# Optimization experiments

Measured on AMD Instinct MI355X. Metric: run time of the kernel, lower is better.

## Reference

```python
import jax, jax.numpy as jnp
import numpy as np

# hypers
R_CUT = 5.0      # 'cutoff radius'
N_MAX = 8        # radial channels
L_MAX = 3        # max spherical-harmonic degree
N_ATOMS = 20000
N_PAIRS = 500000
N_SPECIES = 4    # len(all_species)
N_PSEUDO = 2     # 'alchemical'


def setup_inputs() -> dict:
    key = jax.random.key(0)
    k1, k2, k3, k4, k5 = jax.random.split(key, 5)
    positions = jax.random.normal(k1, (N_ATOMS, 3), dtype=jnp.float32) * 2.0
    centers = jax.random.randint(k2, (N_PAIRS,), 0, N_ATOMS)
    neighbors = jax.random.randint(k3, (N_PAIRS,), 0, N_ATOMS)
    species_idx = jax.random.randint(k4, (N_ATOMS,), 0, N_SPECIES).astype(jnp.int32)
    W_comb = jax.random.normal(k5, (N_PSEUDO, N_SPECIES), dtype=jnp.float32)
    return {"positions": positions, "W_comb": W_comb, "centers": centers,
            "neighbors": neighbors, "species_idx": species_idx}


def _real_spherical_harmonics(x, y, z):
    """Real spherical harmonics Y_lm on unit vectors, l = 0..3.
    Returns list of arrays, each [P, 2l+1] ordered m = -l..l."""
    x2, y2, z2 = x * x, y * y, z * z
    Y0 = jnp.full_like(x, 0.28209479177387814)[:, None]
    c1 = 0.4886025119029199
    Y1 = jnp.stack([c1 * y, c1 * z, c1 * x], axis=-1)
    Y2 = jnp.stack([
        1.0925484305920792 * x * y,
        1.0925484305920792 * y * z,
        0.31539156525252005 * (3.0 * z2 - 1.0),
        1.0925484305920792 * x * z,
        0.5462742152960396 * (x2 - y2),
    ], axis=-1)
    Y3 = jnp.stack([
        0.5900435899266435 * y * (3.0 * x2 - y2),
        2.890611442640554 * x * y * z,
        0.4570457994644658 * y * (5.0 * z2 - 1.0),
        0.3731763325901154 * z * (5.0 * z2 - 3.0),
        0.4570457994644658 * x * (5.0 * z2 - 1.0),
        1.445305721320277 * z * (x2 - y2),
        0.5900435899266435 * x * (x2 - 3.0 * y2),
    ], axis=-1)
    return [Y0, Y1, Y2, Y3]


def reference(positions, W_comb, centers, neighbors, species_idx):
    # pairwise displacement vectors (gather over neighbor list)
    vec = positions[neighbors] - positions[centers]            # [P, 3]
    r = jnp.sqrt((vec * vec).sum(-1) + 1e-12)                  # [P]
    u = vec / r[:, None]                                       # unit vectors

    # smooth radial basis with cosine cutoff (Gaussians on a grid)
    fc = jnp.where(r < R_CUT, 0.5 * (jnp.cos(jnp.pi * r / R_CUT) + 1.0), 0.0)
    cn = jnp.linspace(0.0, R_CUT, N_MAX, dtype=positions.dtype)
    sigma = R_CUT / N_MAX
    radial = jnp.exp(-0.5 * ((r[:, None] - cn) / sigma) ** 2) * fc[:, None]  # [P, n]

    # alchemical combination: one_hot(species_neighbor) @ W_comb.T -> [P, q]
    w = W_comb.T[species_idx[neighbors]]                       # [P, q]
    feat = w[:, :, None] * radial[:, None, :]                  # [P, q, n]

    sph = _real_spherical_harmonics(u[:, 0], u[:, 1], u[:, 2])

    blocks = []
    for Yl in sph:
        # per-pair outer product: [P, 2l+1, q, n]
        exp_l = Yl[:, :, None, None] * feat[:, None, :, :]
        # sum over neighbors j for each center i (scatter-add)
        summed = jax.ops.segment_sum(exp_l, centers, num_segments=N_ATOMS)
        blocks.append(summed.reshape(N_ATOMS, Yl.shape[1], N_PSEUDO * N_MAX))
    # concatenate all l blocks along the component (m) axis: [N_atoms, 16, q*n]
    return jnp.concatenate(blocks, axis=1)
```

## Files before the change

### kernel.cpp

```cpp
#include <hip/hip_runtime.h>
#include <math.h>

#define N_SPECIES 4
#define NMAX      8
#define RCUT      5.0f
#define CAP        64
#define CNT_STRIDE 16


__global__ void prep_kernel(const float* __restrict__ pos,
                            const int*  __restrict__ species,
                            float4* __restrict__ posw, int N) {
    int i = blockIdx.x * blockDim.x + threadIdx.x;
    if (i < N) {
        posw[i] = make_float4(pos[3 * i], pos[3 * i + 1], pos[3 * i + 2],
                              __int_as_float(species[i]));
    }
}


__global__ void build_kernel(const int* __restrict__ centers,
                             const int* __restrict__ neighbors,
                             int* __restrict__ cnt,
                             int* __restrict__ bin, int P) {
    int p = blockIdx.x * blockDim.x + threadIdx.x;
    if (p < P) {
        int c = centers[p];
        int j = neighbors[p];
        int idx = atomicAdd(&cnt[c * CNT_STRIDE], 1);
        if (idx < CAP) bin[c * CAP + idx] = j;
    }
}


__global__ __launch_bounds__(64) void accum_kernel(
        const float4* __restrict__ posw,
        const float*  __restrict__ W,
        const int*    __restrict__ cnt,
        const int*    __restrict__ bin,
        float* __restrict__ out, int N) {
    const int i    = blockIdx.x;
    const int lane = threadIdx.x;

    __shared__ __align__(16) float sY[64][20];
    __shared__ __align__(16) float sF[64][20];

    int payload = bin[i * CAP + lane];
    int ci = cnt[i * CNT_STRIDE];
    if (ci > CAP) ci = CAP;
    int j = payload;
    if ((unsigned)j >= (unsigned)N) j = 0;
    float4 pj = posw[j];
    float4 pi = posw[i];

    float dx = pj.x - pi.x, dy = pj.y - pi.y, dz = pj.z - pi.z;
    float r  = sqrtf(dx * dx + dy * dy + dz * dz + 1e-12f);
    float inv = 1.0f / r;
    float x = dx * inv, y = dy * inv, z = dz * inv;

    float fc = (r < RCUT) ? 0.5f * (cosf(3.14159265358979323846f * (r / RCUT)) + 1.0f)
                          : 0.0f;

    const float Ck[NMAX] = {
        1.0f,          5.2045002e-1f, 7.3369700e-2f, 2.8016300e-3f,
        2.8977800e-5f, 8.1185700e-8f, 6.1609600e-11f, 1.2664166e-14f };
    float rc = (r < RCUT) ? r : RCUT;
    float A  = expf(-1.28f * r * r) * fc;
    float B  = expf(1.82857143f * rc);

    int s = __float_as_int(pj.w);
    float w0 = W[s];
    float w1 = W[N_SPECIES + s];

    float f0[NMAX];
    float pw = A;
    #pragma unroll
    for (int k = 0; k < NMAX; ++k) { f0[k] = pw * Ck[k]; pw *= B; }

    if (lane < ci) {
        float* Fr = sF[lane];
        ((float4*)Fr)[0] = make_float4(w0 * f0[0], w0 * f0[1], w0 * f0[2], w0 * f0[3]);
        ((float4*)Fr)[1] = make_float4(w0 * f0[4], w0 * f0[5], w0 * f0[6], w0 * f0[7]);
        ((float4*)Fr)[2] = make_float4(w1 * f0[0], w1 * f0[1], w1 * f0[2], w1 * f0[3]);
        ((float4*)Fr)[3] = make_float4(w1 * f0[4], w1 * f0[5], w1 * f0[6], w1 * f0[7]);

        float x2 = x * x, y2 = y * y, z2 = z * z;
        float* Yr = sY[lane];
        ((float4*)Yr)[0] = make_float4(
            0.28209479177387814f,
            0.4886025119029199f * y,
            0.4886025119029199f * z,
            0.4886025119029199f * x);
        ((float4*)Yr)[1] = make_float4(
            1.0925484305920792f * x * y,
            1.0925484305920792f * y * z,
            0.31539156525252005f * (3.0f * z2 - 1.0f),
            1.0925484305920792f * x * z);
        ((float4*)Yr)[2] = make_float4(
            0.5462742152960396f * (x2 - y2),
            0.5900435899266435f * y * (3.0f * x2 - y2),
            2.890611442640554f  * x * y * z,
            0.4570457994644658f * y * (5.0f * z2 - 1.0f));
        ((float4*)Yr)[3] = make_float4(
            0.3731763325901154f * z * (5.0f * z2 - 3.0f),
            0.4570457994644658f * x * (5.0f * z2 - 1.0f),
            1.445305721320277f  * z * (x2 - y2),
            0.5900435899266435f * x * (x2 - 3.0f * y2));
    }
    __syncthreads();

    const int m  = lane >> 2;
    const int cg = lane & 3;
    float ax = 0.f, ay = 0.f, az = 0.f, aw = 0.f;
    #pragma unroll 4
    for (int l = 0; l < ci; ++l) {
        float yv = sY[l][m];
        float4 f = *(const float4*)&sF[l][cg * 4];
        ax = fmaf(yv, f.x, ax);
        ay = fmaf(yv, f.y, ay);
        az = fmaf(yv, f.z, az);
        aw = fmaf(yv, f.w, aw);
    }
    float4 o = make_float4(ax, ay, az, aw);
    *(float4*)&out[(size_t)i * 256 + (size_t)lane * 4] = o;
}


extern "C" void kernel_launch(void* const* d_in, const int* in_sizes, int n_in,
                              void* d_out, int out_size, void* d_ws, size_t ws_size,
                              hipStream_t stream) {
    const float* positions = (const float*)d_in[0];
    const float* W_comb    = (const float*)d_in[1];
    const int*   centers   = (const int*)d_in[2];
    const int*   neighbors = (const int*)d_in[3];
    const int*   species   = (const int*)d_in[4];
    float* out = (float*)d_out;

    const int P = in_sizes[2];
    const int N = in_sizes[4];

    float4* posw = (float4*)d_ws;
    int*    cnt  = (int*)(posw + N);
    int*    bin  = cnt + (size_t)N * CNT_STRIDE;

    hipMemsetAsync(cnt, 0, (size_t)N * CNT_STRIDE * sizeof(int), stream);
    prep_kernel<<<(N + 255) / 256, 256, 0, stream>>>(positions, species, posw, N);
    build_kernel<<<(P + 255) / 256, 256, 0, stream>>>(centers, neighbors, cnt, bin, P);
    accum_kernel<<<N, 64, 0, stream>>>(posw, W_comb, cnt, bin, out, N);
}
```

Baseline: 110.9 us.

## Process four atoms per block with 16-neighbor chunks and factored weight accumulation

The accumulation kernel now handles four center atoms per 64-thread block. Each 16-lane group walks its neighbor bin in chunks of 16, staging Y, radial and species weights separately in shared memory. Each lane owns one m component and accumulates all 16 q·n outputs, rebuilding the product from Y·w times radial. The padded counter stride is removed, making the count array dense. The cost is more synchronisation per chunk, and groups whose atom has fewer neighbors idle up to the block's maximum count. The dense counters may also bring back atomic contention on shared cache lines.

```diff
diff --git a/kernel.cpp b/kernel.cpp
--- a/kernel.cpp
+++ b/kernel.cpp
@@ -4,8 +4,7 @@
 #define N_SPECIES 4
 #define NMAX      8
 #define RCUT      5.0f
-#define CAP        64
-#define CNT_STRIDE 16
+#define CAP       64
 
 
 __global__ void prep_kernel(const float* __restrict__ pos,
@@ -27,11 +26,15 @@
     if (p < P) {
         int c = centers[p];
         int j = neighbors[p];
-        int idx = atomicAdd(&cnt[c * CNT_STRIDE], 1);
+        int idx = atomicAdd(&cnt[c], 1);
         if (idx < CAP) bin[c * CAP + idx] = j;
     }
 }
 
+
+#define YSTRIDE (16 * 20 + 8)
+#define RSTRIDE (16 * 8 + 8)
+#define WSTRIDE (16 * 2 + 2)
 
 __global__ __launch_bounds__(64) void accum_kernel(
         const float4* __restrict__ posw,
@@ -39,53 +42,60 @@
         const int*    __restrict__ cnt,
         const int*    __restrict__ bin,
         float* __restrict__ out, int N) {
-    const int i    = blockIdx.x;
     const int lane = threadIdx.x;
+    const int g    = lane >> 4;
+    const int m    = lane & 15;
+    const int a    = blockIdx.x * 4 + g;
+    const int a_safe = (a < N) ? a : (N - 1);
 
-    __shared__ __align__(16) float sY[64][20];
-    __shared__ __align__(16) float sF[64][20];
+    __shared__ __align__(16) float sY[4][YSTRIDE];
+    __shared__ __align__(16) float sR[4][RSTRIDE];
+    __shared__ __align__(16) float sW[4][WSTRIDE];
 
-    int payload = bin[i * CAP + lane];
-    int ci = cnt[i * CNT_STRIDE];
-    if (ci > CAP) ci = CAP;
-    int j = payload;
-    if ((unsigned)j >= (unsigned)N) j = 0;
-    float4 pj = posw[j];
-    float4 pi = posw[i];
+    int ci = 0;
+    if (a < N) { ci = cnt[a]; if (ci > CAP) ci = CAP; }
+    int c0 = __shfl(ci, 0),  c1 = __shfl(ci, 16);
+    int c2 = __shfl(ci, 32), c3 = __shfl(ci, 48);
+    int mc = max(max(c0, c1), max(c2, c3));
 
-    float dx = pj.x - pi.x, dy = pj.y - pi.y, dz = pj.z - pi.z;
-    float r  = sqrtf(dx * dx + dy * dy + dz * dz + 1e-12f);
-    float inv = 1.0f / r;
-    float x = dx * inv, y = dy * inv, z = dz * inv;
+    float4 pi = posw[a_safe];
 
-    float fc = (r < RCUT) ? 0.5f * (cosf(3.14159265358979323846f * (r / RCUT)) + 1.0f)
-                          : 0.0f;
+    float4 acc0 = make_float4(0.f, 0.f, 0.f, 0.f);
+    float4 acc1 = acc0, acc2 = acc0, acc3 = acc0;
 
     const float Ck[NMAX] = {
         1.0f,          5.2045002e-1f, 7.3369700e-2f, 2.8016300e-3f,
         2.8977800e-5f, 8.1185700e-8f, 6.1609600e-11f, 1.2664166e-14f };
-    float rc = (r < RCUT) ? r : RCUT;
-    float A  = expf(-1.28f * r * r) * fc;
-    float B  = expf(1.82857143f * rc);
 
-    int s = __float_as_int(pj.w);
-    float w0 = W[s];
-    float w1 = W[N_SPECIES + s];
+    for (int q = 0; q * 16 < mc; ++q) {
+        int slot = q * 16 + m;
+        bool valid = (slot < ci);
+        int j = bin[a_safe * CAP + slot];
+        if ((unsigned)j >= (unsigned)N) j = 0;
+        float4 pj = posw[j];
 
-    float f0[NMAX];
-    float pw = A;
-    #pragma unroll
-    for (int k = 0; k < NMAX; ++k) { f0[k] = pw * Ck[k]; pw *= B; }
+        float dx = pj.x - pi.x, dy = pj.y - pi.y, dz = pj.z - pi.z;
+        float r  = sqrtf(dx * dx + dy * dy + dz * dz + 1e-12f);
+        float inv = 1.0f / r;
+        float x = dx * inv, y = dy * inv, z = dz * inv;
 
-    if (lane < ci) {
-        float* Fr = sF[lane];
-        ((float4*)Fr)[0] = make_float4(w0 * f0[0], w0 * f0[1], w0 * f0[2], w0 * f0[3]);
-        ((float4*)Fr)[1] = make_float4(w0 * f0[4], w0 * f0[5], w0 * f0[6], w0 * f0[7]);
-        ((float4*)Fr)[2] = make_float4(w1 * f0[0], w1 * f0[1], w1 * f0[2], w1 * f0[3]);
-        ((float4*)Fr)[3] = make_float4(w1 * f0[4], w1 * f0[5], w1 * f0[6], w1 * f0[7]);
+        float fc = (r < RCUT) ? 0.5f * (cosf(3.14159265358979323846f * (r / RCUT)) + 1.0f)
+                              : 0.0f;
+        float rc = (r < RCUT) ? r : RCUT;
+        float A  = expf(-1.28f * r * r) * fc;
+        float B  = expf(1.82857143f * rc);
+
+        int s = __float_as_int(pj.w);
+        float w0 = valid ? W[s] : 0.0f;
+        float w1 = valid ? W[N_SPECIES + s] : 0.0f;
+
+        float f0[NMAX];
+        float pw = A;
+        #pragma unroll
+        for (int k = 0; k < NMAX; ++k) { f0[k] = pw * Ck[k]; pw *= B; }
 
         float x2 = x * x, y2 = y * y, z2 = z * z;
-        float* Yr = sY[lane];
+        float* Yr = &sY[g][m * 20];
         ((float4*)Yr)[0] = make_float4(
             0.28209479177387814f,
             0.4886025119029199f * y,
@@ -106,23 +116,51 @@
             0.4570457994644658f * x * (5.0f * z2 - 1.0f),
             1.445305721320277f  * z * (x2 - y2),
             0.5900435899266435f * x * (x2 - 3.0f * y2));
+
+        float* Rr = &sR[g][m * 8];
+        ((float4*)Rr)[0] = make_float4(f0[0], f0[1], f0[2], f0[3]);
+        ((float4*)Rr)[1] = make_float4(f0[4], f0[5], f0[6], f0[7]);
+
+        float* Wr = &sW[g][m * 2];
+        ((float2*)Wr)[0] = make_float2(w0, w1);
+
+        __syncthreads();
+
+        int tmax = mc - q * 16; if (tmax > 16) tmax = 16;
+        for (int t = 0; t < tmax; ++t) {
+            float  yv = sY[g][t * 20 + m];
+            float2 wv = *(const float2*)&sW[g][t * 2];
+            float4 r0 = *(const float4*)&sR[g][t * 8];
+            float4 r1 = *(const float4*)&sR[g][t * 8 + 4];
+            float yw0 = yv * wv.x;
+            float yw1 = yv * wv.y;
+            acc0.x = fmaf(yw0, r0.x, acc0.x);
+            acc0.y = fmaf(yw0, r0.y, acc0.y);
+            acc0.z = fmaf(yw0, r0.z, acc0.z);
+            acc0.w = fmaf(yw0, r0.w, acc0.w);
+            acc1.x = fmaf(yw0, r1.x, acc1.x);
+            acc1.y = fmaf(yw0, r1.y, acc1.y);
+            acc1.z = fmaf(yw0, r1.z, acc1.z);
+            acc1.w = fmaf(yw0, r1.w, acc1.w);
+            acc2.x = fmaf(yw1, r0.x, acc2.x);
+            acc2.y = fmaf(yw1, r0.y, acc2.y);
+            acc2.z = fmaf(yw1, r0.z, acc2.z);
+            acc2.w = fmaf(yw1, r0.w, acc2.w);
+            acc3.x = fmaf(yw1, r1.x, acc3.x);
+            acc3.y = fmaf(yw1, r1.y, acc3.y);
+            acc3.z = fmaf(yw1, r1.z, acc3.z);
+            acc3.w = fmaf(yw1, r1.w, acc3.w);
+        }
+        __syncthreads();
     }
-    __syncthreads();
 
-    const int m  = lane >> 2;
-    const int cg = lane & 3;
-    float ax = 0.f, ay = 0.f, az = 0.f, aw = 0.f;
-    #pragma unroll 4
-    for (int l = 0; l < ci; ++l) {
-        float yv = sY[l][m];
-        float4 f = *(const float4*)&sF[l][cg * 4];
-        ax = fmaf(yv, f.x, ax);
-        ay = fmaf(yv, f.y, ay);
-        az = fmaf(yv, f.z, az);
-        aw = fmaf(yv, f.w, aw);
+    if (a < N) {
+        float* o = &out[(size_t)a * 256 + (size_t)m * 16];
+        ((float4*)o)[0] = acc0;
+        ((float4*)o)[1] = acc1;
+        ((float4*)o)[2] = acc2;
+        ((float4*)o)[3] = acc3;
     }
-    float4 o = make_float4(ax, ay, az, aw);
-    *(float4*)&out[(size_t)i * 256 + (size_t)lane * 4] = o;
 }
 
 
@@ -141,10 +179,10 @@
 
     float4* posw = (float4*)d_ws;
     int*    cnt  = (int*)(posw + N);
-    int*    bin  = cnt + (size_t)N * CNT_STRIDE;
+    int*    bin  = cnt + N;
 
-    hipMemsetAsync(cnt, 0, (size_t)N * CNT_STRIDE * sizeof(int), stream);
+    hipMemsetAsync(cnt, 0, (size_t)N * sizeof(int), stream);
     prep_kernel<<<(N + 255) / 256, 256, 0, stream>>>(positions, species, posw, N);
     build_kernel<<<(P + 255) / 256, 256, 0, stream>>>(centers, neighbors, cnt, bin, P);
-    accum_kernel<<<N, 64, 0, stream>>>(posw, W_comb, cnt, bin, out, N);
+    accum_kernel<<<(N + 3) / 4, 64, 0, stream>>>(posw, W_comb, cnt, bin, out, N);
 }
```

Result: slower. 115.4 us (+4.0%).

## Fuse prep, bin build and accumulation into one cooperative persistent kernel

Applied to the files above, without the earlier changes.

Replaces the memset plus three kernel launches with a single cooperative kernel that uses grid-wide syncs between the prep, binning and accumulation phases. The accumulation phase becomes persistent: each wave loops over atoms and prefetches the next atom's bin entries. Bins are stored as 16-bit indices and counters are no longer padded, which shrinks workspace traffic but makes the counters contend more and ties correctness to N < 65536. The intent is to remove launch overhead and memory traffic, at the cost of grid.sync latency and block-wide __syncthreads inside the per-atom loop.

```diff
diff --git a/kernel.cpp b/kernel.cpp
--- a/kernel.cpp
+++ b/kernel.cpp
@@ -1,128 +1,156 @@
 #include <hip/hip_runtime.h>
+#include <hip/hip_cooperative_groups.h>
 #include <math.h>
+
+namespace cg = cooperative_groups;
 
 #define N_SPECIES 4
 #define NMAX      8
 #define RCUT      5.0f
-#define CAP        64
-#define CNT_STRIDE 16
+#define CAP       64
+#define NBLOCKS   1536
+#define TPB       128
+#define WPB       (TPB / 64)
 
 
-__global__ void prep_kernel(const float* __restrict__ pos,
-                            const int*  __restrict__ species,
-                            float4* __restrict__ posw, int N) {
-    int i = blockIdx.x * blockDim.x + threadIdx.x;
-    if (i < N) {
+__global__ __launch_bounds__(TPB, 2) void fused_kernel(
+        const float* __restrict__ pos,
+        const float* __restrict__ W,
+        const int*   __restrict__ centers,
+        const int*   __restrict__ neighbors,
+        const int*   __restrict__ species,
+        float4* __restrict__ posw,
+        int*    __restrict__ cnt,
+        unsigned short* __restrict__ bin,
+        float*  __restrict__ out,
+        int N, int P) {
+    cg::grid_group grid = cg::this_grid();
+    const int tid      = blockIdx.x * TPB + threadIdx.x;
+    const int nthreads = gridDim.x * TPB;
+
+    for (int i = tid; i < N; i += nthreads) {
+        cnt[i] = 0;
         posw[i] = make_float4(pos[3 * i], pos[3 * i + 1], pos[3 * i + 2],
                               __int_as_float(species[i]));
     }
-}
+    grid.sync();
 
-
-__global__ void build_kernel(const int* __restrict__ centers,
-                             const int* __restrict__ neighbors,
-                             int* __restrict__ cnt,
-                             int* __restrict__ bin, int P) {
-    int p = blockIdx.x * blockDim.x + threadIdx.x;
-    if (p < P) {
+    for (int p = tid; p < P; p += nthreads) {
         int c = centers[p];
         int j = neighbors[p];
-        int idx = atomicAdd(&cnt[c * CNT_STRIDE], 1);
-        if (idx < CAP) bin[c * CAP + idx] = j;
+        int idx = atomicAdd(&cnt[c], 1);
+        if (idx < CAP) bin[(size_t)c * CAP + idx] = (unsigned short)j;
     }
-}
+    grid.sync();
 
+    const int wave  = threadIdx.x >> 6;
+    const int lane  = threadIdx.x & 63;
+    const int gwave = blockIdx.x * WPB + wave;
+    const int nwaves = gridDim.x * WPB;
+    const int iters  = (N + nwaves - 1) / nwaves;
 
-__global__ __launch_bounds__(64) void accum_kernel(
-        const float4* __restrict__ posw,
-        const float*  __restrict__ W,
-        const int*    __restrict__ cnt,
-        const int*    __restrict__ bin,
-        float* __restrict__ out, int N) {
-    const int i    = blockIdx.x;
-    const int lane = threadIdx.x;
-
-    __shared__ __align__(16) float sY[64][20];
-    __shared__ __align__(16) float sF[64][20];
-
-    int payload = bin[i * CAP + lane];
-    int ci = cnt[i * CNT_STRIDE];
-    if (ci > CAP) ci = CAP;
-    int j = payload;
-    if ((unsigned)j >= (unsigned)N) j = 0;
-    float4 pj = posw[j];
-    float4 pi = posw[i];
-
-    float dx = pj.x - pi.x, dy = pj.y - pi.y, dz = pj.z - pi.z;
-    float r  = sqrtf(dx * dx + dy * dy + dz * dz + 1e-12f);
-    float inv = 1.0f / r;
-    float x = dx * inv, y = dy * inv, z = dz * inv;
-
-    float fc = (r < RCUT) ? 0.5f * (cosf(3.14159265358979323846f * (r / RCUT)) + 1.0f)
-                          : 0.0f;
+    __shared__ __align__(16) float sY[WPB][64][20];
+    __shared__ __align__(16) float sF[WPB][64][20];
 
     const float Ck[NMAX] = {
         1.0f,          5.2045002e-1f, 7.3369700e-2f, 2.8016300e-3f,
         2.8977800e-5f, 8.1185700e-8f, 6.1609600e-11f, 1.2664166e-14f };
-    float rc = (r < RCUT) ? r : RCUT;
-    float A  = expf(-1.28f * r * r) * fc;
-    float B  = expf(1.82857143f * rc);
 
-    int s = __float_as_int(pj.w);
-    float w0 = W[s];
-    float w1 = W[N_SPECIES + s];
+    int a  = gwave;
+    int pay = 0, ci = 0;
+    if (a < N) {
+        pay = bin[(size_t)a * CAP + lane];
+        ci  = cnt[a];
+    }
 
-    float f0[NMAX];
-    float pw = A;
-    #pragma unroll
-    for (int k = 0; k < NMAX; ++k) { f0[k] = pw * Ck[k]; pw *= B; }
+    for (int it = 0; it < iters; ++it) {
+        int a_next = gwave + (it + 1) * nwaves;
+        int pay_n = 0, ci_n = 0;
+        if (it + 1 < iters && a_next < N) {
+            pay_n = bin[(size_t)a_next * CAP + lane];
+            ci_n  = cnt[a_next];
+        }
 
-    if (lane < ci) {
-        float* Fr = sF[lane];
-        ((float4*)Fr)[0] = make_float4(w0 * f0[0], w0 * f0[1], w0 * f0[2], w0 * f0[3]);
-        ((float4*)Fr)[1] = make_float4(w0 * f0[4], w0 * f0[5], w0 * f0[6], w0 * f0[7]);
-        ((float4*)Fr)[2] = make_float4(w1 * f0[0], w1 * f0[1], w1 * f0[2], w1 * f0[3]);
-        ((float4*)Fr)[3] = make_float4(w1 * f0[4], w1 * f0[5], w1 * f0[6], w1 * f0[7]);
+        const bool active = (a < N);
+        int cic = ci; if (cic > CAP) cic = CAP;
 
-        float x2 = x * x, y2 = y * y, z2 = z * z;
-        float* Yr = sY[lane];
-        ((float4*)Yr)[0] = make_float4(
-            0.28209479177387814f,
-            0.4886025119029199f * y,
-            0.4886025119029199f * z,
-            0.4886025119029199f * x);
-        ((float4*)Yr)[1] = make_float4(
-            1.0925484305920792f * x * y,
-            1.0925484305920792f * y * z,
-            0.31539156525252005f * (3.0f * z2 - 1.0f),
-            1.0925484305920792f * x * z);
-        ((float4*)Yr)[2] = make_float4(
-            0.5462742152960396f * (x2 - y2),
-            0.5900435899266435f * y * (3.0f * x2 - y2),
-            2.890611442640554f  * x * y * z,
-            0.4570457994644658f * y * (5.0f * z2 - 1.0f));
-        ((float4*)Yr)[3] = make_float4(
-            0.3731763325901154f * z * (5.0f * z2 - 3.0f),
-            0.4570457994644658f * x * (5.0f * z2 - 1.0f),
-            1.445305721320277f  * z * (x2 - y2),
-            0.5900435899266435f * x * (x2 - 3.0f * y2));
+        if (active && lane < cic) {
+            float4 pi = posw[a];
+            int j = pay;
+            if ((unsigned)j >= (unsigned)N) j = 0;
+            float4 pj = posw[j];
+
+            float dx = pj.x - pi.x, dy = pj.y - pi.y, dz = pj.z - pi.z;
+            float r  = sqrtf(dx * dx + dy * dy + dz * dz + 1e-12f);
+            float inv = 1.0f / r;
+            float x = dx * inv, y = dy * inv, z = dz * inv;
+
+            float fc = (r < RCUT) ? 0.5f * (cosf(3.14159265358979323846f * (r / RCUT)) + 1.0f)
+                                  : 0.0f;
+            float rc = (r < RCUT) ? r : RCUT;
+            float A  = expf(-1.28f * r * r) * fc;
+            float B  = expf(1.82857143f * rc);
+
+            int s = __float_as_int(pj.w);
+            float w0 = W[s];
+            float w1 = W[N_SPECIES + s];
+
+            float f0[NMAX];
+            float pw = A;
+            #pragma unroll
+            for (int k = 0; k < NMAX; ++k) { f0[k] = pw * Ck[k]; pw *= B; }
+
+            float* Fr = sF[wave][lane];
+            ((float4*)Fr)[0] = make_float4(w0 * f0[0], w0 * f0[1], w0 * f0[2], w0 * f0[3]);
+            ((float4*)Fr)[1] = make_float4(w0 * f0[4], w0 * f0[5], w0 * f0[6], w0 * f0[7]);
+            ((float4*)Fr)[2] = make_float4(w1 * f0[0], w1 * f0[1], w1 * f0[2], w1 * f0[3]);
+            ((float4*)Fr)[3] = make_float4(w1 * f0[4], w1 * f0[5], w1 * f0[6], w1 * f0[7]);
+
+            float x2 = x * x, y2 = y * y, z2 = z * z;
+            float* Yr = sY[wave][lane];
+            ((float4*)Yr)[0] = make_float4(
+                0.28209479177387814f,
+                0.4886025119029199f * y,
+                0.4886025119029199f * z,
+                0.4886025119029199f * x);
+            ((float4*)Yr)[1] = make_float4(
+                1.0925484305920792f * x * y,
+                1.0925484305920792f * y * z,
+                0.31539156525252005f * (3.0f * z2 - 1.0f),
+                1.0925484305920792f * x * z);
+            ((float4*)Yr)[2] = make_float4(
+                0.5462742152960396f * (x2 - y2),
+                0.5900435899266435f * y * (3.0f * x2 - y2),
+                2.890611442640554f  * x * y * z,
+                0.4570457994644658f * y * (5.0f * z2 - 1.0f));
+            ((float4*)Yr)[3] = make_float4(
+                0.3731763325901154f * z * (5.0f * z2 - 3.0f),
+                0.4570457994644658f * x * (5.0f * z2 - 1.0f),
+                1.445305721320277f  * z * (x2 - y2),
+                0.5900435899266435f * x * (x2 - 3.0f * y2));
+        }
+        __syncthreads();
+
+        if (active) {
+            const int m  = lane >> 2;
+            const int cg_ = lane & 3;
+            float ax = 0.f, ay = 0.f, az = 0.f, aw = 0.f;
+            #pragma unroll 4
+            for (int l = 0; l < cic; ++l) {
+                float yv = sY[wave][l][m];
+                float4 f = *(const float4*)&sF[wave][l][cg_ * 4];
+                ax = fmaf(yv, f.x, ax);
+                ay = fmaf(yv, f.y, ay);
+                az = fmaf(yv, f.z, az);
+                aw = fmaf(yv, f.w, aw);
+            }
+            float4 o = make_float4(ax, ay, az, aw);
+            *(float4*)&out[(size_t)a * 256 + (size_t)lane * 4] = o;
+        }
+        __syncthreads();
+
+        a = a_next; pay = pay_n; ci = ci_n;
     }
-    __syncthreads();
-
-    const int m  = lane >> 2;
-    const int cg = lane & 3;
-    float ax = 0.f, ay = 0.f, az = 0.f, aw = 0.f;
-    #pragma unroll 4
-    for (int l = 0; l < ci; ++l) {
-        float yv = sY[l][m];
-        float4 f = *(const float4*)&sF[l][cg * 4];
-        ax = fmaf(yv, f.x, ax);
-        ay = fmaf(yv, f.y, ay);
-        az = fmaf(yv, f.z, az);
-        aw = fmaf(yv, f.w, aw);
-    }
-    float4 o = make_float4(ax, ay, az, aw);
-    *(float4*)&out[(size_t)i * 256 + (size_t)lane * 4] = o;
 }
 
 
@@ -136,15 +164,17 @@
     const int*   species   = (const int*)d_in[4];
     float* out = (float*)d_out;
 
-    const int P = in_sizes[2];
-    const int N = in_sizes[4];
+    int P = in_sizes[2];
+    int N = in_sizes[4];
 
-    float4* posw = (float4*)d_ws;
-    int*    cnt  = (int*)(posw + N);
-    int*    bin  = cnt + (size_t)N * CNT_STRIDE;
+    float4*         posw = (float4*)d_ws;
+    int*            cnt  = (int*)(posw + N);
+    unsigned short* bin  = (unsigned short*)(cnt + N);
 
-    hipMemsetAsync(cnt, 0, (size_t)N * CNT_STRIDE * sizeof(int), stream);
-    prep_kernel<<<(N + 255) / 256, 256, 0, stream>>>(positions, species, posw, N);
-    build_kernel<<<(P + 255) / 256, 256, 0, stream>>>(centers, neighbors, cnt, bin, P);
-    accum_kernel<<<N, 64, 0, stream>>>(posw, W_comb, cnt, bin, out, N);
+    void* args[] = { (void*)&positions, (void*)&W_comb, (void*)&centers,
+                     (void*)&neighbors, (void*)&species, (void*)&posw,
+                     (void*)&cnt, (void*)&bin, (void*)&out,
+                     (void*)&N, (void*)&P };
+    hipLaunchCooperativeKernel((const void*)fused_kernel,
+                               dim3(NBLOCKS), dim3(TPB), args, 0, stream);
 }
```

Result: slower. 376.5 us (+239.4%).

## Use bf16 split-precision MFMA for per-atom outer-product accumulation, two atoms per block

Applied to the files above, without the earlier changes.

Replaces the scalar FMA reduction over neighbors with MFMA 16x16x32 bf16 instructions. Each fp32 value is split into hi/lo bf16 parts and three products are summed to keep near-fp32 accuracy. Each 64-thread block now handles two atoms, with 32 neighbors per chunk. The separate memset is folded into the prep kernel and the counter stride padding is dropped. This costs extra packing/unpacking ALU work and two syncs per chunk, and the bf16x3 accuracy is slightly below fp32.

```diff
diff --git a/kernel.cpp b/kernel.cpp
--- a/kernel.cpp
+++ b/kernel.cpp
@@ -4,15 +4,30 @@
 #define N_SPECIES 4
 #define NMAX      8
 #define RCUT      5.0f
-#define CAP        64
-#define CNT_STRIDE 16
+#define CAP       64
+#define KCH       32
+#define LSTRIDE   36
+
+typedef __attribute__((ext_vector_type(8))) short bf16x8;
+typedef __attribute__((ext_vector_type(4))) float f32x4;
+
+union I4B8 { int4 i; bf16x8 s; };
+
+__device__ __forceinline__ unsigned int pack_hilo(float v) {
+    unsigned int bits = __float_as_uint(v);
+    unsigned int hi_f = bits & 0xFFFF0000u;
+    float lo = v - __uint_as_float(hi_f);
+    return (bits >> 16) | (__float_as_uint(lo) & 0xFFFF0000u);
+}
 
 
 __global__ void prep_kernel(const float* __restrict__ pos,
                             const int*  __restrict__ species,
-                            float4* __restrict__ posw, int N) {
+                            float4* __restrict__ posw,
+                            int* __restrict__ cnt, int N) {
     int i = blockIdx.x * blockDim.x + threadIdx.x;
     if (i < N) {
+        cnt[i] = 0;
         posw[i] = make_float4(pos[3 * i], pos[3 * i + 1], pos[3 * i + 2],
                               __int_as_float(species[i]));
     }
@@ -27,7 +42,7 @@
     if (p < P) {
         int c = centers[p];
         int j = neighbors[p];
-        int idx = atomicAdd(&cnt[c * CNT_STRIDE], 1);
+        int idx = atomicAdd(&cnt[c], 1);
         if (idx < CAP) bin[c * CAP + idx] = j;
     }
 }
@@ -39,90 +54,134 @@
         const int*    __restrict__ cnt,
         const int*    __restrict__ bin,
         float* __restrict__ out, int N) {
-    const int i    = blockIdx.x;
     const int lane = threadIdx.x;
-
-    __shared__ __align__(16) float sY[64][20];
-    __shared__ __align__(16) float sF[64][20];
-
-    int payload = bin[i * CAP + lane];
-    int ci = cnt[i * CNT_STRIDE];
-    if (ci > CAP) ci = CAP;
-    int j = payload;
-    if ((unsigned)j >= (unsigned)N) j = 0;
-    float4 pj = posw[j];
-    float4 pi = posw[i];
-
-    float dx = pj.x - pi.x, dy = pj.y - pi.y, dz = pj.z - pi.z;
-    float r  = sqrtf(dx * dx + dy * dy + dz * dz + 1e-12f);
-    float inv = 1.0f / r;
-    float x = dx * inv, y = dy * inv, z = dz * inv;
-
-    float fc = (r < RCUT) ? 0.5f * (cosf(3.14159265358979323846f * (r / RCUT)) + 1.0f)
-                          : 0.0f;
+    const int h = lane >> 5;
+    const int k = lane & 31;
+    const int a0 = blockIdx.x * 2;
+    const int aA = a0 + h;
+    const int a_safe = (aA < N) ? aA : (N - 1);
+
+    __shared__ unsigned int sY[2][16][LSTRIDE];
+    __shared__ unsigned int sF[2][16][LSTRIDE];
+
+    int ciA = 0;
+    if (aA < N) { ciA = cnt[aA]; if (ciA > CAP) ciA = CAP; }
+    int ci0 = __shfl(ciA, 0);
+    int ci1 = __shfl(ciA, 32);
+    int mc = max(ci0, ci1);
+    int nch = (mc + KCH - 1) / KCH;
+
+    f32x4 acc0 = {0.f, 0.f, 0.f, 0.f};
+    f32x4 acc1 = {0.f, 0.f, 0.f, 0.f};
 
     const float Ck[NMAX] = {
         1.0f,          5.2045002e-1f, 7.3369700e-2f, 2.8016300e-3f,
         2.8977800e-5f, 8.1185700e-8f, 6.1609600e-11f, 1.2664166e-14f };
-    float rc = (r < RCUT) ? r : RCUT;
-    float A  = expf(-1.28f * r * r) * fc;
-    float B  = expf(1.82857143f * rc);
-
-    int s = __float_as_int(pj.w);
-    float w0 = W[s];
-    float w1 = W[N_SPECIES + s];
-
-    float f0[NMAX];
-    float pw = A;
-    #pragma unroll
-    for (int k = 0; k < NMAX; ++k) { f0[k] = pw * Ck[k]; pw *= B; }
-
-    if (lane < ci) {
-        float* Fr = sF[lane];
-        ((float4*)Fr)[0] = make_float4(w0 * f0[0], w0 * f0[1], w0 * f0[2], w0 * f0[3]);
-        ((float4*)Fr)[1] = make_float4(w0 * f0[4], w0 * f0[5], w0 * f0[6], w0 * f0[7]);
-        ((float4*)Fr)[2] = make_float4(w1 * f0[0], w1 * f0[1], w1 * f0[2], w1 * f0[3]);
-        ((float4*)Fr)[3] = make_float4(w1 * f0[4], w1 * f0[5], w1 * f0[6], w1 * f0[7]);
+
+    const int quad = lane >> 4;
+    const int col  = lane & 15;
+
+    float4 pi = posw[a_safe];
+
+    for (int q = 0; q < nch; ++q) {
+        int slot = q * KCH + k;
+        bool valid = (aA < N) && (slot < ciA);
+        int j = bin[a_safe * CAP + slot];
+        if ((unsigned)j >= (unsigned)N) j = 0;
+        float4 pj = posw[j];
+
+        float dx = pj.x - pi.x, dy = pj.y - pi.y, dz = pj.z - pi.z;
+        float r  = sqrtf(dx * dx + dy * dy + dz * dz + 1e-12f);
+        float inv = 1.0f / r;
+        float x = dx * inv, y = dy * inv, z = dz * inv;
+
+        float fc = (r < RCUT) ? 0.5f * (cosf(3.14159265358979323846f * (r / RCUT)) + 1.0f)
+                              : 0.0f;
+        float rc = (r < RCUT) ? r : RCUT;
+        float A  = expf(-1.28f * r * r) * fc;
+        float B  = expf(1.82857143f * rc);
+
+        int s = __float_as_int(pj.w);
+        float w0 = valid ? W[s] : 0.0f;
+        float w1 = valid ? W[N_SPECIES + s] : 0.0f;
+
+        float f0[NMAX];
+        float pw = A;
+        #pragma unroll
+        for (int kk = 0; kk < NMAX; ++kk) { f0[kk] = pw * Ck[kk]; pw *= B; }
 
         float x2 = x * x, y2 = y * y, z2 = z * z;
-        float* Yr = sY[lane];
-        ((float4*)Yr)[0] = make_float4(
-            0.28209479177387814f,
-            0.4886025119029199f * y,
-            0.4886025119029199f * z,
-            0.4886025119029199f * x);
-        ((float4*)Yr)[1] = make_float4(
-            1.0925484305920792f * x * y,
-            1.0925484305920792f * y * z,
-            0.31539156525252005f * (3.0f * z2 - 1.0f),
-            1.0925484305920792f * x * z);
-        ((float4*)Yr)[2] = make_float4(
-            0.5462742152960396f * (x2 - y2),
-            0.5900435899266435f * y * (3.0f * x2 - y2),
-            2.890611442640554f  * x * y * z,
-            0.4570457994644658f * y * (5.0f * z2 - 1.0f));
-        ((float4*)Yr)[3] = make_float4(
-            0.3731763325901154f * z * (5.0f * z2 - 3.0f),
-            0.4570457994644658f * x * (5.0f * z2 - 1.0f),
-            1.445305721320277f  * z * (x2 - y2),
-            0.5900435899266435f * x * (x2 - 3.0f * y2));
-    }
-    __syncthreads();
-
-    const int m  = lane >> 2;
-    const int cg = lane & 3;
-    float ax = 0.f, ay = 0.f, az = 0.f, aw = 0.f;
-    #pragma unroll 4
-    for (int l = 0; l < ci; ++l) {
-        float yv = sY[l][m];
-        float4 f = *(const float4*)&sF[l][cg * 4];
-        ax = fmaf(yv, f.x, ax);
-        ay = fmaf(yv, f.y, ay);
-        az = fmaf(yv, f.z, az);
-        aw = fmaf(yv, f.w, aw);
-    }
-    float4 o = make_float4(ax, ay, az, aw);
-    *(float4*)&out[(size_t)i * 256 + (size_t)lane * 4] = o;
+        float Y[16];
+        Y[0]  = 0.28209479177387814f;
+        Y[1]  = 0.4886025119029199f * y;
+        Y[2]  = 0.4886025119029199f * z;
+        Y[3]  = 0.4886025119029199f * x;
+        Y[4]  = 1.0925484305920792f * x * y;
+        Y[5]  = 1.0925484305920792f * y * z;
+        Y[6]  = 0.31539156525252005f * (3.0f * z2 - 1.0f);
+        Y[7]  = 1.0925484305920792f * x * z;
+        Y[8]  = 0.5462742152960396f * (x2 - y2);
+        Y[9]  = 0.5900435899266435f * y * (3.0f * x2 - y2);
+        Y[10] = 2.890611442640554f  * x * y * z;
+        Y[11] = 0.4570457994644658f * y * (5.0f * z2 - 1.0f);
+        Y[12] = 0.3731763325901154f * z * (5.0f * z2 - 3.0f);
+        Y[13] = 0.4570457994644658f * x * (5.0f * z2 - 1.0f);
+        Y[14] = 1.445305721320277f  * z * (x2 - y2);
+        Y[15] = 0.5900435899266435f * x * (x2 - 3.0f * y2);
+
+        #pragma unroll
+        for (int m = 0; m < 16; ++m) sY[h][m][k] = pack_hilo(Y[m]);
+        #pragma unroll
+        for (int c = 0; c < NMAX; ++c) {
+            sF[h][c][k]        = pack_hilo(w0 * f0[c]);
+            sF[h][c + NMAX][k] = pack_hilo(w1 * f0[c]);
+        }
+        __syncthreads();
+
+        #pragma unroll
+        for (int at = 0; at < 2; ++at) {
+            uint4 ya = *(const uint4*)&sY[at][col][quad * 8];
+            uint4 yb = *(const uint4*)&sY[at][col][quad * 8 + 4];
+            uint4 fa = *(const uint4*)&sF[at][col][quad * 8];
+            uint4 fb = *(const uint4*)&sF[at][col][quad * 8 + 4];
+
+            I4B8 Ah, Al, Bh, Bl;
+            Ah.i = make_int4((ya.x & 0xFFFF) | (ya.y << 16),
+                             (ya.z & 0xFFFF) | (ya.w << 16),
+                             (yb.x & 0xFFFF) | (yb.y << 16),
+                             (yb.z & 0xFFFF) | (yb.w << 16));
+            Al.i = make_int4((ya.x >> 16) | (ya.y & 0xFFFF0000u),
+                             (ya.z >> 16) | (ya.w & 0xFFFF0000u),
+                             (yb.x >> 16) | (yb.y & 0xFFFF0000u),
+                             (yb.z >> 16) | (yb.w & 0xFFFF0000u));
+            Bh.i = make_int4((fa.x & 0xFFFF) | (fa.y << 16),
+                             (fa.z & 0xFFFF) | (fa.w << 16),
+                             (fb.x & 0xFFFF) | (fb.y << 16),
+                             (fb.z & 0xFFFF) | (fb.w << 16));
+            Bl.i = make_int4((fa.x >> 16) | (fa.y & 0xFFFF0000u),
+                             (fa.z >> 16) | (fa.w & 0xFFFF0000u),
+                             (fb.x >> 16) | (fb.y & 0xFFFF0000u),
+                             (fb.z >> 16) | (fb.w & 0xFFFF0000u));
+
+            f32x4 acc = (at == 0) ? acc0 : acc1;
+            acc = __builtin_amdgcn_mfma_f32_16x16x32_bf16(Ah.s, Bh.s, acc, 0, 0, 0);
+            acc = __builtin_amdgcn_mfma_f32_16x16x32_bf16(Ah.s, Bl.s, acc, 0, 0, 0);
+            acc = __builtin_amdgcn_mfma_f32_16x16x32_bf16(Al.s, Bh.s, acc, 0, 0, 0);
+            if (at == 0) acc0 = acc; else acc1 = acc;
+        }
+        __syncthreads();
+    }
+
+    if (a0 < N) {
+        #pragma unroll
+        for (int rr = 0; rr < 4; ++rr)
+            out[(size_t)a0 * 256 + (quad * 4 + rr) * 16 + col] = acc0[rr];
+    }
+    if (a0 + 1 < N) {
+        #pragma unroll
+        for (int rr = 0; rr < 4; ++rr)
+            out[(size_t)(a0 + 1) * 256 + (quad * 4 + rr) * 16 + col] = acc1[rr];
+    }
 }
 
 
@@ -141,10 +200,9 @@
 
     float4* posw = (float4*)d_ws;
     int*    cnt  = (int*)(posw + N);
-    int*    bin  = cnt + (size_t)N * CNT_STRIDE;
-
-    hipMemsetAsync(cnt, 0, (size_t)N * CNT_STRIDE * sizeof(int), stream);
-    prep_kernel<<<(N + 255) / 256, 256, 0, stream>>>(positions, species, posw, N);
+    int*    bin  = cnt + N;
+
+    prep_kernel<<<(N + 255) / 256, 256, 0, stream>>>(positions, species, posw, cnt, N);
     build_kernel<<<(P + 255) / 256, 256, 0, stream>>>(centers, neighbors, cnt, bin, P);
-    accum_kernel<<<N, 64, 0, stream>>>(posw, W_comb, cnt, bin, out, N);
-}
+    accum_kernel<<<(N + 1) / 2, 64, 0, stream>>>(posw, W_comb, cnt, bin, out, N);
+}
```

New measurement: 109.8 us. About the same (-1.1%).
